# Kernel optimization log

Measured on AMD Instinct MI355X. Metric: run time of the kernel, lower is better.

## Reference

```python
import jax, jax.numpy as jnp
import numpy as np


def setup_inputs() -> dict:
    key = jax.random.key(0)
    k1, k2 = jax.random.split(key)
    support_features = jax.random.normal(k1, (1000, 5, 512), dtype=jnp.float32)
    query_features = jax.random.normal(k2, (5000, 512), dtype=jnp.float32)
    return {"support_features": support_features, "query_features": query_features, "use_cosine": 1}


def reference(support_features, query_features, use_cosine):
    # Preprocess: mean-center over (classes, shots), then L2-normalize per vector.
    mean = jnp.mean(support_features, axis=(0, 1), keepdims=True)  # [1,1,D]
    s = support_features - mean                                    # [C,S,D]
    q = query_features - mean[0]                                   # [Q,D]
    s = s / jnp.linalg.norm(s, axis=2, keepdims=True)
    q = q / jnp.linalg.norm(q, axis=1, keepdims=True)
    if use_cosine:
        # cosine sims without materializing [C,Q,S,D]; einsum fuses the dot.
        sims = jnp.einsum('csd,qd->cqs', s, q)   # [C,Q,S]
        best = jnp.max(sims, axis=2)             # [C,Q] best shot per class
        return jnp.argmax(best, axis=0)          # [Q] predicted class
    else:
        # euclidean cdist(query[Q,D], support[C,S,D]) -> [C,Q,S]
        d2 = (jnp.sum(q * q, axis=1)[None, :, None]
              + jnp.sum(s * s, axis=2)[:, None, :]
              - 2.0 * jnp.einsum('csd,qd->cqs', s, q))
        dist = jnp.sqrt(jnp.maximum(d2, 0.0))
        best = jnp.min(dist, axis=2)
        return jnp.argmin(best, axis=0)
```

## Files before the change

kernel.cpp:

```cpp
#include <hip/hip_runtime.h>
#include <stdint.h>

#define D     512
#define NSUP  5000
#define NQRY  5000
#define NPAD  5120
#define MEAN_BLOCKS 100
#define ROWS_PER_MEAN_BLOCK 50
#define SCALE 512.0f

#define OFF_SHI     0
#define OFF_SLO     5242880
#define OFF_QHI     10485760
#define OFF_QLO     15728640
#define OFF_PARTIAL 20971520
#define OFF_MEAN    21176320
#define OFF_KEYS    21178368

#define SH_SHI   0
#define SH_SLO   32768
#define SH_QHI   65536
#define SH_QLO   98304
#define SH_KL    131072
#define SH_TOTAL (131072 + 2048)

typedef _Float16 half4v __attribute__((ext_vector_type(4)));
typedef _Float16 half8v __attribute__((ext_vector_type(8)));
typedef float    f32x4  __attribute__((ext_vector_type(4)));

__device__ __forceinline__ unsigned long long pack_key(float v, int sidx) {
    unsigned u = __float_as_uint(v);
    u = (u & 0x80000000u) ? ~u : (u | 0x80000000u);
    return ((unsigned long long)u << 32) | (unsigned)(0xFFFFFFFFu - (unsigned)sidx);
}

__device__ __forceinline__ void gload16(const void* g, void* l) {
    __builtin_amdgcn_global_load_lds(
        (const __attribute__((address_space(1))) unsigned int*)g,
        (__attribute__((address_space(3))) unsigned int*)l, 16, 0, 0);
}

__global__ void k_partial_mean(const float* __restrict__ sup, float* __restrict__ partial) {
    const int col = threadIdx.x;
    const int b   = blockIdx.x;
    const int r0  = b * ROWS_PER_MEAN_BLOCK;
    float acc = 0.0f;
    #pragma unroll 5
    for (int r = 0; r < ROWS_PER_MEAN_BLOCK; ++r)
        acc += sup[(size_t)(r0 + r) * D + col];
    partial[b * D + col] = acc;
}

__global__ void k_mean_init(const float* __restrict__ partial, float* __restrict__ mean,
                            unsigned long long* __restrict__ keys) {
    const int col = threadIdx.x;
    float acc = 0.0f;
    #pragma unroll 4
    for (int b = 0; b < MEAN_BLOCKS; ++b) acc += partial[b * D + col];
    mean[col] = acc * (1.0f / (float)NSUP);
    for (int i = col; i < NSUP; i += 512) keys[i] = 0ull;
}

__global__ void k_split(const float* __restrict__ sup, const float* __restrict__ qry,
                        const float* __restrict__ mean,
                        _Float16* __restrict__ shi, _Float16* __restrict__ slo,
                        _Float16* __restrict__ qhi, _Float16* __restrict__ qlo) {
    const int t    = threadIdx.x;
    const int rloc = t >> 7;
    const int tc   = t & 127;
    const int b    = (int)blockIdx.x * 4 + rloc;
    const float* src; _Float16 *dhi, *dlo; int valid;
    if (b < NPAD) { src = sup + (size_t)b * D;
                    dhi = shi + (size_t)b * D; dlo = slo + (size_t)b * D; valid = (b < NSUP); }
    else          { int r = b - NPAD; src = qry + (size_t)r * D;
                    dhi = qhi + (size_t)r * D; dlo = qlo + (size_t)r * D; valid = (r < NQRY); }
    __shared__ float red[8];
    if (!valid) {
        half4v z = {};
        *(half4v*)(dhi + tc * 4) = z;
        *(half4v*)(dlo + tc * 4) = z;
        return;
    }
    float4 v = *(const float4*)(src + tc * 4);
    float4 m = *(const float4*)(mean + tc * 4);
    v.x -= m.x; v.y -= m.y; v.z -= m.z; v.w -= m.w;
    float ss = v.x * v.x + v.y * v.y + v.z * v.z + v.w * v.w;
    #pragma unroll
    for (int off = 32; off > 0; off >>= 1) ss += __shfl_down(ss, off, 64);
    if ((t & 63) == 0) red[t >> 6] = ss;
    __syncthreads();
    const float rn = SCALE / sqrtf(red[rloc * 2] + red[rloc * 2 + 1]);
    float sv[4] = {v.x * rn, v.y * rn, v.z * rn, v.w * rn};
    half4v h, l;
    #pragma unroll
    for (int i = 0; i < 4; ++i) {
        _Float16 hh = (_Float16)sv[i];
        h[i] = hh;
        l[i] = (_Float16)(sv[i] - (float)hh);
    }
    *(half4v*)(dhi + tc * 4) = h;
    *(half4v*)(dlo + tc * 4) = l;
}

__launch_bounds__(512, 2)
__global__ void k_main(const _Float16* __restrict__ shi, const _Float16* __restrict__ slo,
                       const _Float16* __restrict__ qhi, const _Float16* __restrict__ qlo,
                       unsigned long long* __restrict__ keys) {
    extern __shared__ char smem[];
    char* lshi = smem + SH_SHI;
    char* lslo = smem + SH_SLO;
    char* lqhi = smem + SH_QHI;
    char* lqlo = smem + SH_QLO;
    unsigned long long* kl = (unsigned long long*)(smem + SH_KL);

    const int tid  = threadIdx.x;
    const int lane = tid & 63;
    const int wv   = tid >> 6;
    const int q0   = blockIdx.x * 256;
    const int s0   = blockIdx.y * 256;
    const int wr   = wv >> 2;
    const int wc   = wv & 3;

    if (tid < 256) kl[tid] = 0ull;

    const int srow = wv * 16 + (lane >> 2);
    const int sl0  = ((lane & 3) ^ ((lane >> 3) & 3)) * 16;
    const size_t gA0 = (size_t)(s0 + srow) * 1024 + sl0;
    const size_t gB0 = (size_t)(q0 + srow) * 1024 + sl0;
    const char* pShi = (const char*)shi; const char* pSlo = (const char*)slo;
    const char* pQhi = (const char*)qhi; const char* pQlo = (const char*)qlo;
    const int dst0 = wv * 1024;
    const int dst1 = 8192 + wv * 1024;

    const int l15 = lane & 15;
    const int kg  = lane >> 4;
    const int swz = (kg ^ ((l15 >> 1) & 3)) * 16;
    const int foA = (wr * 128 + l15) * 64 + swz;
    const int foB = (wc * 64  + l15) * 64 + swz;

    f32x4 acc[8][4] = {};

#define BAR()    asm volatile("s_barrier" ::: "memory")
#define WAITV0() asm volatile("s_waitcnt vmcnt(0)" ::: "memory")
#define WAITL()  asm volatile("s_waitcnt lgkmcnt(0)" ::: "memory")

#define ST2(P, KT, K2) do { const size_t kb_ = (size_t)(KT) * 64;           \
        if ((K2) == 0) {                                                    \
            gload16(pShi + gA0 + kb_,          lshi + (P) * 16384 + dst0);  \
            gload16(pShi + gA0 + 131072 + kb_, lshi + (P) * 16384 + dst1);  \
        } else if ((K2) == 1) {                                             \
            gload16(pSlo + gA0 + kb_,          lslo + (P) * 16384 + dst0);  \
            gload16(pSlo + gA0 + 131072 + kb_, lslo + (P) * 16384 + dst1);  \
        } else if ((K2) == 2) {                                             \
            gload16(pQhi + gB0 + kb_,          lqhi + (P) * 16384 + dst0);  \
            gload16(pQhi + gB0 + 131072 + kb_, lqhi + (P) * 16384 + dst1);  \
        } else {                                                            \
            gload16(pQlo + gB0 + kb_,          lqlo + (P) * 16384 + dst0);  \
            gload16(pQlo + gB0 + 131072 + kb_, lqlo + (P) * 16384 + dst1);  \
        } } while (0)

#define RD_A2(P, FA, AI) do {                                               \
        ah[AI]   = *(const half8v*)(lshi + (P)*16384 + foA + (FA)*1024);    \
        al[AI]   = *(const half8v*)(lslo + (P)*16384 + foA + (FA)*1024);    \
        ah[AI+1] = *(const half8v*)(lshi + (P)*16384 + foA + (FA+1)*1024);  \
        al[AI+1] = *(const half8v*)(lslo + (P)*16384 + foA + (FA+1)*1024);  \
    } while (0)

#define RD_B(P, QB, BH, BL) do { _Pragma("unroll")                          \
        for (int j_ = 0; j_ < 2; ++j_) {                                    \
            BH[j_] = *(const half8v*)(lqhi + (P)*16384 + foB + ((QB)*2 + j_)*1024); \
            BL[j_] = *(const half8v*)(lqlo + (P)*16384 + foB + ((QB)*2 + j_)*1024); \
        } } while (0)

#define MMA12(R0, AI, C0, BH, BL) do {                                      \
        __builtin_amdgcn_s_setprio(1);                                      \
        _Pragma("unroll")                                                   \
        for (int i_ = 0; i_ < 2; ++i_)                                      \
        { _Pragma("unroll")                                                 \
          for (int j_ = 0; j_ < 2; ++j_) {                                  \
            f32x4* a_ = &acc[(R0) + i_][(C0) + j_];                         \
            *a_ = __builtin_amdgcn_mfma_f32_16x16x32_f16(ah[(AI)+i_], BH[j_], *a_, 0, 0, 0); \
            *a_ = __builtin_amdgcn_mfma_f32_16x16x32_f16(ah[(AI)+i_], BL[j_], *a_, 0, 0, 0); \
            *a_ = __builtin_amdgcn_mfma_f32_16x16x32_f16(al[(AI)+i_], BH[j_], *a_, 0, 0, 0); \
          } }                                                               \
        __builtin_amdgcn_s_setprio(0);                                      \
        __builtin_amdgcn_sched_barrier(0);                                  \
    } while (0)

    ST2(0, 0, 0); ST2(0, 0, 1); ST2(0, 0, 2); ST2(0, 0, 3);
    WAITV0();
    BAR();

    for (int t = 0; t < 16; ++t) {
        const int P  = t & 1;
        const int Pn = P ^ 1;
        const int tn = (t + 1 < 16) ? (t + 1) : 0;
        half8v ah[4], al[4], bh0[2], bl0[2], bh1[2], bl1[2];

        RD_A2(P, 0, 0); RD_B(P, 0, bh0, bl0); ST2(Pn, tn, 0);
        BAR(); WAITL(); MMA12(0, 0, 0, bh0, bl0); BAR();
        RD_A2(P, 2, 2); ST2(Pn, tn, 1);
        BAR(); WAITL(); MMA12(2, 2, 0, bh0, bl0); BAR();
        RD_B(P, 1, bh1, bl1); ST2(Pn, tn, 2);
        BAR(); WAITL(); MMA12(0, 0, 2, bh1, bl1); BAR();
        ST2(Pn, tn, 3);
        BAR(); MMA12(2, 2, 2, bh1, bl1); BAR();
        RD_A2(P, 4, 0);
        BAR(); WAITL(); MMA12(4, 0, 0, bh0, bl0); BAR();
        RD_A2(P, 6, 2);
        BAR(); WAITL(); MMA12(6, 2, 0, bh0, bl0); BAR();
        BAR(); MMA12(4, 0, 2, bh1, bl1); BAR();
        BAR(); MMA12(6, 2, 2, bh1, bl1);
        WAITV0();
        BAR();
    }

#undef MMA12
#undef RD_B
#undef RD_A2
#undef ST2

    #pragma unroll
    for (int fb = 0; fb < 4; ++fb) {
        unsigned long long best = 0ull;
        #pragma unroll
        for (int fa = 0; fa < 8; ++fa)
            #pragma unroll
            for (int r = 0; r < 4; ++r) {
                const int s = s0 + wr * 128 + fa * 16 + kg * 4 + r;
                if (s < NSUP) {
                    unsigned long long k = pack_key(acc[fa][fb][r], s);
                    if (k > best) best = k;
                }
            }
        unsigned long long o = __shfl_xor(best, 16, 64); if (o > best) best = o;
        o = __shfl_xor(best, 32, 64);                    if (o > best) best = o;
        if (kg == 0) atomicMax(&kl[wc * 64 + fb * 16 + l15], best);
    }
    __syncthreads();
    if (tid < 256) {
        const int q = q0 + tid;
        if (q < NQRY && kl[tid] != 0ull) atomicMax(&keys[q], kl[tid]);
    }
}

__global__ void k_decode(const unsigned long long* __restrict__ keys, int* __restrict__ out) {
    const int q = blockIdx.x * 256 + threadIdx.x;
    if (q < NQRY) {
        unsigned sidx = 0xFFFFFFFFu - (unsigned)(keys[q] & 0xFFFFFFFFull);
        out[q] = (int)(sidx / 5u);
    }
}

extern "C" void kernel_launch(void* const* d_in, const int* in_sizes, int n_in,
                              void* d_out, int out_size, void* d_ws, size_t ws_size,
                              hipStream_t stream) {
    const float* sup = (const float*)d_in[0];
    const float* qry = (const float*)d_in[1];
    int* out = (int*)d_out;

    char* ws = (char*)d_ws;
    _Float16* shi = (_Float16*)(ws + OFF_SHI);
    _Float16* slo = (_Float16*)(ws + OFF_SLO);
    _Float16* qhi = (_Float16*)(ws + OFF_QHI);
    _Float16* qlo = (_Float16*)(ws + OFF_QLO);
    float* partial = (float*)(ws + OFF_PARTIAL);
    float* mean    = (float*)(ws + OFF_MEAN);
    unsigned long long* keys = (unsigned long long*)(ws + OFF_KEYS);

    static bool attr_set = false;
    if (!attr_set) {
        (void)hipFuncSetAttribute((const void*)k_main,
                                  hipFuncAttributeMaxDynamicSharedMemorySize, SH_TOTAL);
        attr_set = true;
    }

    k_partial_mean<<<MEAN_BLOCKS, 512, 0, stream>>>(sup, partial);
    k_mean_init<<<1, 512, 0, stream>>>(partial, mean, keys);
    k_split<<<(2 * NPAD) / 4, 512, 0, stream>>>(sup, qry, mean, shi, slo, qhi, qlo);
    dim3 grid(NPAD / 256, NPAD / 256);
    k_main<<<grid, 512, SH_TOTAL, stream>>>(shi, slo, qhi, qlo, keys);
    k_decode<<<(NQRY + 255) / 256, 256, 0, stream>>>(keys, out);
}
```

Baseline: 165.4 us.

## Shrink main GEMM tile to 128x256 with 32x32 MFMA and smaller LDS

Restructures the split-fp16 similarity GEMM to use 128-support by 256-query tiles, a K-step of 16 halves (32 iterations), and 32x32x16 MFMA instructions instead of 16x16x32. LDS use drops from about 130KB to 50KB and launch bounds ask for 4 blocks per CU, aiming for higher occupancy and fewer barriers per MFMA group. The trade-off is more global traffic, since support tiles are reused across fewer queries and twice as many blocks are launched. The simpler single-stage double buffer may expose more load latency per iteration.

Result: slower. 187.2 us (+13.2%).

```diff
diff --git a/kernel.cpp b/kernel.cpp
--- a/kernel.cpp
+++ b/kernel.cpp
@@ -18,15 +18,15 @@
 #define OFF_KEYS    21178368
 
 #define SH_SHI   0
-#define SH_SLO   32768
-#define SH_QHI   65536
-#define SH_QLO   98304
-#define SH_KL    131072
-#define SH_TOTAL (131072 + 2048)
-
-typedef _Float16 half4v __attribute__((ext_vector_type(4)));
-typedef _Float16 half8v __attribute__((ext_vector_type(8)));
-typedef float    f32x4  __attribute__((ext_vector_type(4)));
+#define SH_SLO   8192
+#define SH_QHI   16384
+#define SH_QLO   32768
+#define SH_KL    49152
+#define SH_TOTAL 51200
+
+typedef _Float16 half4v  __attribute__((ext_vector_type(4)));
+typedef _Float16 half8v  __attribute__((ext_vector_type(8)));
+typedef float    f32x16  __attribute__((ext_vector_type(16)));
 
 __device__ __forceinline__ unsigned long long pack_key(float v, int sidx) {
     unsigned u = __float_as_uint(v);
@@ -102,7 +102,7 @@
     *(half4v*)(dlo + tc * 4) = l;
 }
 
-__launch_bounds__(512, 2)
+__launch_bounds__(512, 4)
 __global__ void k_main(const _Float16* __restrict__ shi, const _Float16* __restrict__ slo,
                        const _Float16* __restrict__ qhi, const _Float16* __restrict__ qlo,
                        unsigned long long* __restrict__ keys) {
@@ -117,131 +117,102 @@
     const int lane = tid & 63;
     const int wv   = tid >> 6;
     const int q0   = blockIdx.x * 256;
-    const int s0   = blockIdx.y * 256;
+    const int s0   = blockIdx.y * 128;
     const int wr   = wv >> 2;
     const int wc   = wv & 3;
 
     if (tid < 256) kl[tid] = 0ull;
 
-    const int srow = wv * 16 + (lane >> 2);
-    const int sl0  = ((lane & 3) ^ ((lane >> 3) & 3)) * 16;
-    const size_t gA0 = (size_t)(s0 + srow) * 1024 + sl0;
-    const size_t gB0 = (size_t)(q0 + srow) * 1024 + sl0;
-    const char* pShi = (const char*)shi; const char* pSlo = (const char*)slo;
+    const int row_q = tid >> 1;
+    const int ps_q  = (tid & 1) ^ ((row_q >> 1) & 1);
+    const size_t gQ = (size_t)(q0 + row_q) * 1024 + ps_q * 16;
+    const int row_s = (wv & 3) * 32 + (lane >> 1);
+    const int ps_s  = (lane & 1) ^ ((row_s >> 1) & 1);
+    const size_t gS = (size_t)(s0 + row_s) * 1024 + ps_s * 16;
+    const char* pS  = (wv < 4) ? (const char*)shi : (const char*)slo;
+    char* ldsS      = (wv < 4) ? lshi : lslo;
     const char* pQhi = (const char*)qhi; const char* pQlo = (const char*)qlo;
-    const int dst0 = wv * 1024;
-    const int dst1 = 8192 + wv * 1024;
-
-    const int l15 = lane & 15;
-    const int kg  = lane >> 4;
-    const int swz = (kg ^ ((l15 >> 1) & 3)) * 16;
-    const int foA = (wr * 128 + l15) * 64 + swz;
-    const int foB = (wc * 64  + l15) * 64 + swz;
-
-    f32x4 acc[8][4] = {};
+    const int dstS = (wv & 3) * 1024;
+    const int dstQ = wv * 1024;
+
+    const int r31 = lane & 31;
+    const int khl = lane >> 5;
+    const int psr = (khl ^ ((r31 >> 1) & 1)) * 16;
+    const int foA = (wr * 64 + r31) * 32 + psr;
+    const int foB = (wc * 64 + r31) * 32 + psr;
+
+    f32x16 acc[2][2] = {};
 
 #define BAR()    asm volatile("s_barrier" ::: "memory")
 #define WAITV0() asm volatile("s_waitcnt vmcnt(0)" ::: "memory")
 #define WAITL()  asm volatile("s_waitcnt lgkmcnt(0)" ::: "memory")
 
-#define ST2(P, KT, K2) do { const size_t kb_ = (size_t)(KT) * 64;           \
-        if ((K2) == 0) {                                                    \
-            gload16(pShi + gA0 + kb_,          lshi + (P) * 16384 + dst0);  \
-            gload16(pShi + gA0 + 131072 + kb_, lshi + (P) * 16384 + dst1);  \
-        } else if ((K2) == 1) {                                             \
-            gload16(pSlo + gA0 + kb_,          lslo + (P) * 16384 + dst0);  \
-            gload16(pSlo + gA0 + 131072 + kb_, lslo + (P) * 16384 + dst1);  \
-        } else if ((K2) == 2) {                                             \
-            gload16(pQhi + gB0 + kb_,          lqhi + (P) * 16384 + dst0);  \
-            gload16(pQhi + gB0 + 131072 + kb_, lqhi + (P) * 16384 + dst1);  \
-        } else {                                                            \
-            gload16(pQlo + gB0 + kb_,          lqlo + (P) * 16384 + dst0);  \
-            gload16(pQlo + gB0 + 131072 + kb_, lqlo + (P) * 16384 + dst1);  \
-        } } while (0)
-
-#define RD_A2(P, FA, AI) do {                                               \
-        ah[AI]   = *(const half8v*)(lshi + (P)*16384 + foA + (FA)*1024);    \
-        al[AI]   = *(const half8v*)(lslo + (P)*16384 + foA + (FA)*1024);    \
-        ah[AI+1] = *(const half8v*)(lshi + (P)*16384 + foA + (FA+1)*1024);  \
-        al[AI+1] = *(const half8v*)(lslo + (P)*16384 + foA + (FA+1)*1024);  \
-    } while (0)
-
-#define RD_B(P, QB, BH, BL) do { _Pragma("unroll")                          \
-        for (int j_ = 0; j_ < 2; ++j_) {                                    \
-            BH[j_] = *(const half8v*)(lqhi + (P)*16384 + foB + ((QB)*2 + j_)*1024); \
-            BL[j_] = *(const half8v*)(lqlo + (P)*16384 + foB + ((QB)*2 + j_)*1024); \
-        } } while (0)
-
-#define MMA12(R0, AI, C0, BH, BL) do {                                      \
-        __builtin_amdgcn_s_setprio(1);                                      \
-        _Pragma("unroll")                                                   \
-        for (int i_ = 0; i_ < 2; ++i_)                                      \
-        { _Pragma("unroll")                                                 \
-          for (int j_ = 0; j_ < 2; ++j_) {                                  \
-            f32x4* a_ = &acc[(R0) + i_][(C0) + j_];                         \
-            *a_ = __builtin_amdgcn_mfma_f32_16x16x32_f16(ah[(AI)+i_], BH[j_], *a_, 0, 0, 0); \
-            *a_ = __builtin_amdgcn_mfma_f32_16x16x32_f16(ah[(AI)+i_], BL[j_], *a_, 0, 0, 0); \
-            *a_ = __builtin_amdgcn_mfma_f32_16x16x32_f16(al[(AI)+i_], BH[j_], *a_, 0, 0, 0); \
-          } }                                                               \
-        __builtin_amdgcn_s_setprio(0);                                      \
-        __builtin_amdgcn_sched_barrier(0);                                  \
-    } while (0)
-
-    ST2(0, 0, 0); ST2(0, 0, 1); ST2(0, 0, 2); ST2(0, 0, 3);
+    gload16(pS   + gS, ldsS + dstS);
+    gload16(pQhi + gQ, lqhi + dstQ);
+    gload16(pQlo + gQ, lqlo + dstQ);
     WAITV0();
     BAR();
 
-    for (int t = 0; t < 16; ++t) {
-        const int P  = t & 1;
-        const int Pn = P ^ 1;
-        const int tn = (t + 1 < 16) ? (t + 1) : 0;
-        half8v ah[4], al[4], bh0[2], bl0[2], bh1[2], bl1[2];
-
-        RD_A2(P, 0, 0); RD_B(P, 0, bh0, bl0); ST2(Pn, tn, 0);
-        BAR(); WAITL(); MMA12(0, 0, 0, bh0, bl0); BAR();
-        RD_A2(P, 2, 2); ST2(Pn, tn, 1);
-        BAR(); WAITL(); MMA12(2, 2, 0, bh0, bl0); BAR();
-        RD_B(P, 1, bh1, bl1); ST2(Pn, tn, 2);
-        BAR(); WAITL(); MMA12(0, 0, 2, bh1, bl1); BAR();
-        ST2(Pn, tn, 3);
-        BAR(); MMA12(2, 2, 2, bh1, bl1); BAR();
-        RD_A2(P, 4, 0);
-        BAR(); WAITL(); MMA12(4, 0, 0, bh0, bl0); BAR();
-        RD_A2(P, 6, 2);
-        BAR(); WAITL(); MMA12(6, 2, 0, bh0, bl0); BAR();
-        BAR(); MMA12(4, 0, 2, bh1, bl1); BAR();
-        BAR(); MMA12(6, 2, 2, bh1, bl1);
+    for (int t = 0; t < 32; ++t) {
+        const int P = t & 1;
+        half8v ah[2], al[2], bh[2], bl[2];
+        #pragma unroll
+        for (int ab = 0; ab < 2; ++ab) {
+            ah[ab] = *(const half8v*)(lshi + P * 4096 + foA + ab * 1024);
+            al[ab] = *(const half8v*)(lslo + P * 4096 + foA + ab * 1024);
+        }
+        #pragma unroll
+        for (int qb = 0; qb < 2; ++qb) {
+            bh[qb] = *(const half8v*)(lqhi + P * 8192 + foB + qb * 1024);
+            bl[qb] = *(const half8v*)(lqlo + P * 8192 + foB + qb * 1024);
+        }
+        if (t < 31) {
+            const size_t kb = (size_t)(t + 1) * 32;
+            gload16(pS   + gS + kb, ldsS + (P ^ 1) * 4096 + dstS);
+            gload16(pQhi + gQ + kb, lqhi + (P ^ 1) * 8192 + dstQ);
+            gload16(pQlo + gQ + kb, lqlo + (P ^ 1) * 8192 + dstQ);
+        }
+        BAR();
+        WAITL();
+        __builtin_amdgcn_s_setprio(1);
+        #pragma unroll
+        for (int ab = 0; ab < 2; ++ab)
+            #pragma unroll
+            for (int qb = 0; qb < 2; ++qb) {
+                acc[ab][qb] = __builtin_amdgcn_mfma_f32_32x32x16_f16(ah[ab], bh[qb], acc[ab][qb], 0, 0, 0);
+                acc[ab][qb] = __builtin_amdgcn_mfma_f32_32x32x16_f16(ah[ab], bl[qb], acc[ab][qb], 0, 0, 0);
+                acc[ab][qb] = __builtin_amdgcn_mfma_f32_32x32x16_f16(al[ab], bh[qb], acc[ab][qb], 0, 0, 0);
+            }
+        __builtin_amdgcn_s_setprio(0);
+        __builtin_amdgcn_sched_barrier(0);
         WAITV0();
         BAR();
     }
 
-#undef MMA12
-#undef RD_B
-#undef RD_A2
-#undef ST2
-
     #pragma unroll
-    for (int fb = 0; fb < 4; ++fb) {
+    for (int qb = 0; qb < 2; ++qb) {
         unsigned long long best = 0ull;
         #pragma unroll
-        for (int fa = 0; fa < 8; ++fa)
+        for (int ab = 0; ab < 2; ++ab)
             #pragma unroll
-            for (int r = 0; r < 4; ++r) {
-                const int s = s0 + wr * 128 + fa * 16 + kg * 4 + r;
+            for (int rg = 0; rg < 16; ++rg) {
+                const int s = s0 + wr * 64 + ab * 32 + (rg & 3) + 8 * (rg >> 2) + 4 * khl;
                 if (s < NSUP) {
-                    unsigned long long k = pack_key(acc[fa][fb][r], s);
+                    unsigned long long k = pack_key(acc[ab][qb][rg], s);
                     if (k > best) best = k;
                 }
             }
-        unsigned long long o = __shfl_xor(best, 16, 64); if (o > best) best = o;
-        o = __shfl_xor(best, 32, 64);                    if (o > best) best = o;
-        if (kg == 0) atomicMax(&kl[wc * 64 + fb * 16 + l15], best);
+        unsigned long long o = __shfl_xor(best, 32, 64); if (o > best) best = o;
+        if (lane < 32) atomicMax(&kl[wc * 64 + qb * 32 + r31], best);
     }
     __syncthreads();
     if (tid < 256) {
         const int q = q0 + tid;
         if (q < NQRY && kl[tid] != 0ull) atomicMax(&keys[q], kl[tid]);
     }
+#undef BAR
+#undef WAITV0
+#undef WAITL
 }
 
 __global__ void k_decode(const unsigned long long* __restrict__ keys, int* __restrict__ out) {
@@ -278,7 +249,7 @@
     k_partial_mean<<<MEAN_BLOCKS, 512, 0, stream>>>(sup, partial);
     k_mean_init<<<1, 512, 0, stream>>>(partial, mean, keys);
     k_split<<<(2 * NPAD) / 4, 512, 0, stream>>>(sup, qry, mean, shi, slo, qhi, qlo);
-    dim3 grid(NPAD / 256, NPAD / 256);
+    dim3 grid(NPAD / 256, NPAD / 128);
     k_main<<<grid, 512, SH_TOTAL, stream>>>(shi, slo, qhi, qlo, keys);
     k_decode<<<(NQRY + 255) / 256, 256, 0, stream>>>(keys, out);
 }
```

## Restructure split-fp16 MFMA loop into three phases with partial vmcnt waits

Applied to the files above, without the earlier changes.

Replaces the eight fine-grained read/MMA phases, each separated by barriers, with three larger phases. Each phase loads a full set of A or B fragments and runs 32 MFMAs covering the hi*hi, lo*hi and hi*lo products. The full `vmcnt(0)` drain and `lgkmcnt` waits become counted `vmcnt(6)`/`vmcnt(4)` waits, and the global-to-LDS issue order is rearranged so lo-part prefetches can stay in flight across the iteration boundary. This is meant to cut barrier and memory-wait stalls and overlap loads with compute, at the cost of more live fragment registers and a fragile dependence on exact load counts.

After: 163.9 us. About the same (-0.9%).

```diff
diff --git a/kernel.cpp b/kernel.cpp
--- a/kernel.cpp
+++ b/kernel.cpp
@@ -141,8 +141,8 @@
     f32x4 acc[8][4] = {};
 
 #define BAR()    asm volatile("s_barrier" ::: "memory")
-#define WAITV0() asm volatile("s_waitcnt vmcnt(0)" ::: "memory")
-#define WAITL()  asm volatile("s_waitcnt lgkmcnt(0)" ::: "memory")
+#define WAITV6() asm volatile("s_waitcnt vmcnt(6)" ::: "memory")
+#define WAITV4() asm volatile("s_waitcnt vmcnt(4)" ::: "memory")
 
 #define ST2(P, KT, K2) do { const size_t kb_ = (size_t)(KT) * 64;           \
         if ((K2) == 0) {                                                    \
@@ -159,65 +159,59 @@
             gload16(pQlo + gB0 + 131072 + kb_, lqlo + (P) * 16384 + dst1);  \
         } } while (0)
 
-#define RD_A2(P, FA, AI) do {                                               \
-        ah[AI]   = *(const half8v*)(lshi + (P)*16384 + foA + (FA)*1024);    \
-        al[AI]   = *(const half8v*)(lslo + (P)*16384 + foA + (FA)*1024);    \
-        ah[AI+1] = *(const half8v*)(lshi + (P)*16384 + foA + (FA+1)*1024);  \
-        al[AI+1] = *(const half8v*)(lslo + (P)*16384 + foA + (FA+1)*1024);  \
-    } while (0)
-
-#define RD_B(P, QB, BH, BL) do { _Pragma("unroll")                          \
-        for (int j_ = 0; j_ < 2; ++j_) {                                    \
-            BH[j_] = *(const half8v*)(lqhi + (P)*16384 + foB + ((QB)*2 + j_)*1024); \
-            BL[j_] = *(const half8v*)(lqlo + (P)*16384 + foB + ((QB)*2 + j_)*1024); \
-        } } while (0)
-
-#define MMA12(R0, AI, C0, BH, BL) do {                                      \
+#define MMA32(AV, BV) do {                                                  \
         __builtin_amdgcn_s_setprio(1);                                      \
         _Pragma("unroll")                                                   \
-        for (int i_ = 0; i_ < 2; ++i_)                                      \
+        for (int fa_ = 0; fa_ < 8; ++fa_)                                   \
         { _Pragma("unroll")                                                 \
-          for (int j_ = 0; j_ < 2; ++j_) {                                  \
-            f32x4* a_ = &acc[(R0) + i_][(C0) + j_];                         \
-            *a_ = __builtin_amdgcn_mfma_f32_16x16x32_f16(ah[(AI)+i_], BH[j_], *a_, 0, 0, 0); \
-            *a_ = __builtin_amdgcn_mfma_f32_16x16x32_f16(ah[(AI)+i_], BL[j_], *a_, 0, 0, 0); \
-            *a_ = __builtin_amdgcn_mfma_f32_16x16x32_f16(al[(AI)+i_], BH[j_], *a_, 0, 0, 0); \
+          for (int fb_ = 0; fb_ < 4; ++fb_) {                               \
+            acc[fa_][fb_] = __builtin_amdgcn_mfma_f32_16x16x32_f16(         \
+                AV[fa_], BV[fb_], acc[fa_][fb_], 0, 0, 0);                  \
           } }                                                               \
         __builtin_amdgcn_s_setprio(0);                                      \
         __builtin_amdgcn_sched_barrier(0);                                  \
     } while (0)
 
-    ST2(0, 0, 0); ST2(0, 0, 1); ST2(0, 0, 2); ST2(0, 0, 3);
-    WAITV0();
+    ST2(0, 0, 0); ST2(0, 0, 2); ST2(0, 0, 1); ST2(0, 0, 3);
+    WAITV4();
     BAR();
 
     for (int t = 0; t < 16; ++t) {
         const int P  = t & 1;
         const int Pn = P ^ 1;
-        const int tn = (t + 1 < 16) ? (t + 1) : 0;
-        half8v ah[4], al[4], bh0[2], bl0[2], bh1[2], bl1[2];
-
-        RD_A2(P, 0, 0); RD_B(P, 0, bh0, bl0); ST2(Pn, tn, 0);
-        BAR(); WAITL(); MMA12(0, 0, 0, bh0, bl0); BAR();
-        RD_A2(P, 2, 2); ST2(Pn, tn, 1);
-        BAR(); WAITL(); MMA12(2, 2, 0, bh0, bl0); BAR();
-        RD_B(P, 1, bh1, bl1); ST2(Pn, tn, 2);
-        BAR(); WAITL(); MMA12(0, 0, 2, bh1, bl1); BAR();
+        const int tn = (t + 1) & 15;
+        half8v ah[8], al[8], bh[4], bl[4];
+
+        #pragma unroll
+        for (int f = 0; f < 8; ++f)
+            ah[f] = *(const half8v*)(lshi + P * 16384 + foA + f * 1024);
+        #pragma unroll
+        for (int j = 0; j < 4; ++j)
+            bh[j] = *(const half8v*)(lqhi + P * 16384 + foB + j * 1024);
+        ST2(Pn, tn, 0);
+        ST2(Pn, tn, 2);
+        MMA32(ah, bh);
+        WAITV6();
+        BAR();
+
+        #pragma unroll
+        for (int f = 0; f < 8; ++f)
+            al[f] = *(const half8v*)(lslo + P * 16384 + foA + f * 1024);
+        ST2(Pn, tn, 1);
+        MMA32(al, bh);
+        WAITV6();
+        BAR();
+
+        #pragma unroll
+        for (int j = 0; j < 4; ++j)
+            bl[j] = *(const half8v*)(lqlo + P * 16384 + foB + j * 1024);
         ST2(Pn, tn, 3);
-        BAR(); MMA12(2, 2, 2, bh1, bl1); BAR();
-        RD_A2(P, 4, 0);
-        BAR(); WAITL(); MMA12(4, 0, 0, bh0, bl0); BAR();
-        RD_A2(P, 6, 2);
-        BAR(); WAITL(); MMA12(6, 2, 0, bh0, bl0); BAR();
-        BAR(); MMA12(4, 0, 2, bh1, bl1); BAR();
-        BAR(); MMA12(6, 2, 2, bh1, bl1);
-        WAITV0();
+        MMA32(ah, bl);
+        WAITV4();
         BAR();
     }
 
-#undef MMA12
-#undef RD_B
-#undef RD_A2
+#undef MMA32
 #undef ST2
 
     #pragma unroll
@@ -242,6 +236,9 @@
         const int q = q0 + tid;
         if (q < NQRY && kl[tid] != 0ull) atomicMax(&keys[q], kl[tid]);
     }
+#undef BAR
+#undef WAITV6
+#undef WAITV4
 }
 
 __global__ void k_decode(const unsigned long long* __restrict__ keys, int* __restrict__ out) {
```
